# Performance work log

Hardware: AMD Instinct MI355X
Metric: run time of the kernel (lower is better)

Reference implementation:

```python
import jax, jax.numpy as jnp
import numpy as np

B = 256      # n_batch
N = 256      # n_x
RHO = 1.0    # control['rho']
N_ITERS = 50 # control['max_iters'], run fixed (no early stop) for determinism


def setup_inputs() -> dict:
    key = jax.random.key(0)
    k1, k2 = jax.random.split(key)
    # Build a well-conditioned symmetric PSD Q (QP requires Q PSD)
    Araw = jax.random.normal(k1, (B, N, N), dtype=jnp.float32)
    Q = jnp.einsum('bij,bkj->bik', Araw, Araw) / N + jnp.eye(N, dtype=jnp.float32)
    p = jax.random.normal(k2, (B, N, 1), dtype=jnp.float32)
    lb = -jnp.ones((B, N, 1), dtype=jnp.float32)
    ub = jnp.ones((B, N, 1), dtype=jnp.float32)
    return {"Q": Q, "p": p, "lb": lb, "ub": ub}


def reference(Q, p, lb, ub):
    n = Q.shape[1]
    # M = Q + rho*I, LU-factored once (rho fixed: adaptive_rho=False)
    M = Q + RHO * jnp.eye(n, dtype=Q.dtype)
    lu, piv = jax.vmap(jax.scipy.linalg.lu_factor)(M)
    solve = jax.vmap(lambda l, pv, r: jax.scipy.linalg.lu_solve((l, pv), r))

    x0 = jnp.zeros_like(p)
    z0 = jnp.zeros_like(p)
    u0 = jnp.zeros_like(p)

    def step(carry, _):
        x, z, u = carry
        rhs = -p + RHO * (z - u)            # [B,N,1]
        x = solve(lu, piv, rhs)             # batched LU solve
        z = jnp.clip(x + u, lb, ub)         # box projection (max with lb, min with ub)
        u = u + (x - z)                     # dual update
        return (x, z, u), None

    (x, z, u), _ = jax.lax.scan(step, (x0, z0, u0), None, length=N_ITERS)
    # scale=False => D=1, so sol x = D*x = x (unroll=True path returns x)
    return x
```

## Files before the change

### kernel.cpp

```cpp
#include <hip/hip_runtime.h>


#define NX     256
#define NITER  50
#define TRIF   33280
#define NTILE  2080
#define NTHR   1024

__device__ __forceinline__ int rowoff(int r) {
    int M = r >> 2, s = r & 3;
    return 4 * (M + 1) * ((M << 1) + s);
}

__launch_bounds__(NTHR, 1)
__global__ void boxqp_blk_kernel(const float* __restrict__ Q,
                                 const float* __restrict__ p,
                                 const float* __restrict__ lb,
                                 const float* __restrict__ ub,
                                 float* __restrict__ out)
{
    extern __shared__ char smem_raw[];
    float*  tri  = (float*)smem_raw;
    float4* tri4 = (float4*)tri;
    float4* P4   = (float4*)(tri + TRIF);
    float4* W4   = P4 + NX;
    float*  vbuf = (float*)(W4 + NX);
    unsigned char* lut = (unsigned char*)(vbuf + 272);

    const int t = threadIdx.x;
    const int b = blockIdx.x;
    const size_t qbase = ((size_t)b) << 16;

    if (t < 64) {
        int base = (t * (t + 1)) >> 1;
        for (int c = 0; c <= t; ++c) lut[base + c] = (unsigned char)t;
    }
    __syncthreads();

    for (int tile = t; tile < NTILE; tile += NTHR) {
        int rb = lut[tile];
        int cb = tile - ((rb * (rb + 1)) >> 1);
        int r0 = rb << 2, j0 = cb << 2;
        int q0 = ((rb + 1) * (rb << 1)) + cb, step = rb + 1;
        if (rb != cb) {
            #pragma unroll
            for (int s2 = 0; s2 < 4; ++s2) {
                float4 v = *(const float4*)(Q + qbase + (size_t)(r0 + s2) * NX + j0);
                tri4[q0 + s2 * step] = v;
            }
        } else {
            #pragma unroll
            for (int s2 = 0; s2 < 4; ++s2) {
                int rr = r0 + s2;
                float4 v = *(const float4*)(Q + qbase + (size_t)rr * NX + j0);
                float4 tq;
                tq.x = (j0 + 0 > rr) ? 0.f : (v.x + ((j0 + 0 == rr) ? 1.f : 0.f));
                tq.y = (j0 + 1 > rr) ? 0.f : (v.y + ((j0 + 1 == rr) ? 1.f : 0.f));
                tq.z = (j0 + 2 > rr) ? 0.f : (v.z + ((j0 + 2 == rr) ? 1.f : 0.f));
                tq.w = (j0 + 3 > rr) ? 0.f : (v.w + ((j0 + 3 == rr) ? 1.f : 0.f));
                tri4[q0 + s2 * step] = tq;
            }
        }
    }
    __syncthreads();

    for (int kb = 0; kb < 64; ++kb) {
        const int k0 = kb << 2;

        if (t < NX) {
            int i = t;
            float4 pv;
            if (i >= k0 + 4) {
                pv = tri4[(rowoff(i) >> 2) + kb];
            } else {
                float v0, v1, v2, v3;
                #pragma unroll
                for (int m = 0; m < 4; ++m) {
                    int km = k0 + m;
                    float vv = (km <= i) ? tri[rowoff(i) + km] : tri[rowoff(km) + i];
                    if (m == 0) v0 = vv; else if (m == 1) v1 = vv;
                    else if (m == 2) v2 = vv; else v3 = vv;
                }
                pv = make_float4(v0, v1, v2, v3);
            }
            P4[i] = pv;
        }
        __syncthreads();

        float S[4][4];
        {
            #pragma unroll
            for (int m = 0; m < 4; ++m) {
                float4 pr = P4[k0 + m];
                S[m][0] = pr.x; S[m][1] = pr.y; S[m][2] = pr.z; S[m][3] = pr.w;
            }
            #pragma unroll
            for (int kk = 0; kk < 4; ++kk) {
                float inv = 1.0f / S[kk][kk];
                #pragma unroll
                for (int a2 = 0; a2 < 4; ++a2) {
                    if (a2 == kk) continue;
                    #pragma unroll
                    for (int b2 = 0; b2 < 4; ++b2) {
                        if (b2 == kk) continue;
                        S[a2][b2] -= S[a2][kk] * S[kk][b2] * inv;
                    }
                }
                #pragma unroll
                for (int a2 = 0; a2 < 4; ++a2) {
                    if (a2 == kk) continue;
                    S[a2][kk] *= inv;
                    S[kk][a2] *= inv;
                }
                S[kk][kk] = -inv;
            }
        }
        if (t < NX) {
            float4 pr = P4[t];
            float4 w;
            w.x = -(pr.x * S[0][0] + pr.y * S[1][0] + pr.z * S[2][0] + pr.w * S[3][0]);
            w.y = -(pr.x * S[0][1] + pr.y * S[1][1] + pr.z * S[2][1] + pr.w * S[3][1]);
            w.z = -(pr.x * S[0][2] + pr.y * S[1][2] + pr.z * S[2][2] + pr.w * S[3][2]);
            w.w = -(pr.x * S[0][3] + pr.y * S[1][3] + pr.z * S[2][3] + pr.w * S[3][3]);
            W4[t] = w;
        }
        __syncthreads();

        for (int tile = t; tile < NTILE; tile += NTHR) {
            int rb = lut[tile];
            int cb = tile - ((rb * (rb + 1)) >> 1);
            int r0 = rb << 2;
            int q0 = ((rb + 1) * (rb << 1)) + cb, step = rb + 1;
            if (rb == kb) {
                if (cb == kb) {
                    #pragma unroll
                    for (int s2 = 0; s2 < 4; ++s2)
                        tri4[q0 + s2 * step] = make_float4(S[s2][0], S[s2][1], S[s2][2], S[s2][3]);
                } else {
                    int j0 = cb << 2;
                    #pragma unroll
                    for (int s2 = 0; s2 < 4; ++s2) {
                        float4 v;
                        v.x = ((const float*)(W4 + j0 + 0))[s2];
                        v.y = ((const float*)(W4 + j0 + 1))[s2];
                        v.z = ((const float*)(W4 + j0 + 2))[s2];
                        v.w = ((const float*)(W4 + j0 + 3))[s2];
                        tri4[q0 + s2 * step] = v;
                    }
                }
            } else if (cb == kb) {
                #pragma unroll
                for (int s2 = 0; s2 < 4; ++s2)
                    tri4[q0 + s2 * step] = W4[r0 + s2];
            } else {
                int j0 = cb << 2;
                float4 Pc0 = P4[j0 + 0], Pc1 = P4[j0 + 1], Pc2 = P4[j0 + 2], Pc3 = P4[j0 + 3];
                #pragma unroll
                for (int s2 = 0; s2 < 4; ++s2) {
                    float4 wr = W4[r0 + s2];
                    float4 tq = tri4[q0 + s2 * step];
                    tq.x -= wr.x * Pc0.x + wr.y * Pc0.y + wr.z * Pc0.z + wr.w * Pc0.w;
                    tq.y -= wr.x * Pc1.x + wr.y * Pc1.y + wr.z * Pc1.z + wr.w * Pc1.w;
                    tq.z -= wr.x * Pc2.x + wr.y * Pc2.y + wr.z * Pc2.z + wr.w * Pc2.w;
                    tq.w -= wr.x * Pc3.x + wr.y * Pc3.y + wr.z * Pc3.z + wr.w * Pc3.w;
                    tri4[q0 + s2 * step] = tq;
                }
            }
        }
        __syncthreads();
    }

    const int r  = t >> 2;
    const int q4 = t & 3;
    const int jc = q4 << 6;
    float mr[64];
    {
        const int offr = rowoff(r);
        #pragma unroll
        for (int jj = 0; jj < 64; ++jj) {
            int j = jc + jj;
            int addr = (j <= r) ? (offr + j) : (rowoff(j) + r);
            mr[jj] = tri[addr];
        }
    }

    const int gb = (b << 8) + r;
    const float pi = p[gb], lbi = lb[gb], ubi = ub[gb];
    const int vw = r + ((r >> 6) << 2);

    float x = 0.f, z = 0.f, u = 0.f;
    __syncthreads();
    for (int it = 0; it < NITER; ++it) {
        if (q4 == 0) vbuf[vw] = (u + pi) - z;
        __syncthreads();
        const float4* vb4 = (const float4*)(vbuf + q4 * 68);
        float a0 = 0.f, a1 = 0.f, a2 = 0.f, a3 = 0.f;
        #pragma unroll
        for (int m = 0; m < 16; ++m) {
            float4 v = vb4[m];
            a0 += mr[4 * m + 0] * v.x;
            a1 += mr[4 * m + 1] * v.y;
            a2 += mr[4 * m + 2] * v.z;
            a3 += mr[4 * m + 3] * v.w;
        }
        float s = (a0 + a1) + (a2 + a3);
        s += __shfl_xor(s, 1);
        s += __shfl_xor(s, 2);
        x = s;
        float xu = x + u;
        z = fminf(fmaxf(xu, lbi), ubi);
        u = xu - z;
        __syncthreads();
    }

    if (q4 == 0) out[gb] = x;
}

extern "C" void kernel_launch(void* const* d_in, const int* in_sizes, int n_in,
                              void* d_out, int out_size, void* d_ws, size_t ws_size,
                              hipStream_t stream) {
    const float* Q  = (const float*)d_in[0];
    const float* p  = (const float*)d_in[1];
    const float* lb = (const float*)d_in[2];
    const float* ub = (const float*)d_in[3];
    float* out = (float*)d_out;

    const size_t shmem = (size_t)TRIF * 4 + NX * 16 + NX * 16 + 272 * 4 + NTILE;
    (void)hipFuncSetAttribute((const void*)boxqp_blk_kernel,
                              hipFuncAttributeMaxDynamicSharedMemorySize,
                              (int)shmem);

    hipLaunchKernelGGL(boxqp_blk_kernel, dim3(256), dim3(NTHR), shmem, stream,
                       Q, p, lb, ub, out);
}
```

Measured before the change: 362.0 us.

## Swizzle packed-triangle LDS layout and split ADMM matvec across four row chunks

Rewrites the kernel with an XOR-swizzled packed lower-triangular layout in LDS to cut bank conflicts. Tile coordinates are now computed per thread with sqrt instead of a lookup table. The pivot panel is loaded by all 1024 threads into a transposed PT buffer, and W is stored both row-wise and transposed. The iteration matvec now reads the inverse directly from LDS, with each of four thread groups handling a 64-column chunk and partial sums reduced through LDS. This replaces the 64-register cached row, lowering register pressure but adding LDS traffic and an extra reduction step in every iteration.

Result: slower. 1.111 ms (+206.8%).

```diff
diff --git a/kernel.cpp b/kernel.cpp
--- a/kernel.cpp
+++ b/kernel.cpp
@@ -3,217 +3,260 @@
 
 #define NX     256
 #define NITER  50
-#define TRIF   33280
-#define NTILE  2080
 #define NTHR   1024
 
-__device__ __forceinline__ int rowoff(int r) {
-    int M = r >> 2, s = r & 3;
-    return 4 * (M + 1) * ((M << 1) + s);
-}
-
-__launch_bounds__(NTHR, 1)
-__global__ void boxqp_blk_kernel(const float* __restrict__ Q,
-                                 const float* __restrict__ p,
-                                 const float* __restrict__ lb,
-                                 const float* __restrict__ ub,
-                                 float* __restrict__ out)
+#define OFF_PT  33280
+#define OFF_W4  (OFF_PT + 4 * 264)
+#define OFF_WT  (OFF_W4 + 1024)
+#define LDS_F   (OFF_WT + 4 * 264)
+
+__host__ __device__ constexpr int rowoff(int r) {
+    return 4 * ((r >> 2) + 1) * (((r >> 2) << 1) + (r & 3));
+}
+__device__ __forceinline__ int triq(int q) { return q ^ ((q >> 3) & 7); }
+__device__ __forceinline__ int triF(int a) { return a ^ ((a >> 3) & 28); }
+
+__device__ __forceinline__ int tile_rb(int s) {
+    int r = (int)((sqrtf(8.0f * (float)s + 1.0f) - 1.0f) * 0.5f);
+    while ((r + 1) * (r + 2) / 2 <= s) ++r;
+    while (r * (r + 1) / 2 > s) --r;
+    return r;
+}
+
+template <int J0>
+__device__ __forceinline__ float chunk_upper_f(const float* tri, const float* vb, int rr) {
+    float a0 = 0.f, a1 = 0.f, a2 = 0.f, a3 = 0.f;
+    #pragma unroll
+    for (int jj = 0; jj < 64; jj += 4) {
+        a0 += tri[triF(rowoff(J0 + jj + 0) + rr)] * vb[J0 + jj + 0];
+        a1 += tri[triF(rowoff(J0 + jj + 1) + rr)] * vb[J0 + jj + 1];
+        a2 += tri[triF(rowoff(J0 + jj + 2) + rr)] * vb[J0 + jj + 2];
+        a3 += tri[triF(rowoff(J0 + jj + 3) + rr)] * vb[J0 + jj + 3];
+    }
+    return (a0 + a1) + (a2 + a3);
+}
+template <int J0>
+__device__ __forceinline__ float chunk_mixed_f(const float* tri, const float* vb, int rr) {
+    const int ror = rowoff(rr);
+    float a0 = 0.f, a1 = 0.f, a2 = 0.f, a3 = 0.f;
+    #pragma unroll
+    for (int jj = 0; jj < 64; jj += 4) {
+        {   const int j = J0 + jj + 0;
+            a0 += tri[triF((j <= rr) ? (ror + j) : (rowoff(j) + rr))] * vb[j]; }
+        {   const int j = J0 + jj + 1;
+            a1 += tri[triF((j <= rr) ? (ror + j) : (rowoff(j) + rr))] * vb[j]; }
+        {   const int j = J0 + jj + 2;
+            a2 += tri[triF((j <= rr) ? (ror + j) : (rowoff(j) + rr))] * vb[j]; }
+        {   const int j = J0 + jj + 3;
+            a3 += tri[triF((j <= rr) ? (ror + j) : (rowoff(j) + rr))] * vb[j]; }
+    }
+    return (a0 + a1) + (a2 + a3);
+}
+__device__ __forceinline__ float chunk_lower_f(const float4* tri4, const float* vb,
+                                               int rowq, int q4) {
+    const int qb = rowq + (q4 << 4);
+    const float* vbp = vb + (q4 << 6);
+    float a0 = 0.f, a1 = 0.f, a2 = 0.f, a3 = 0.f;
+    #pragma unroll
+    for (int m = 0; m < 16; ++m) {
+        const float4 A = tri4[triq(qb + m)];
+        const float4 V = *(const float4*)(vbp + 4 * m);
+        a0 += A.x * V.x; a1 += A.y * V.y; a2 += A.z * V.z; a3 += A.w * V.w;
+    }
+    return (a0 + a1) + (a2 + a3);
+}
+
+__global__ void __launch_bounds__(NTHR, 1)
+boxqp_r10_kernel(const float* __restrict__ Q,
+                 const float* __restrict__ p,
+                 const float* __restrict__ lb,
+                 const float* __restrict__ ub,
+                 float* __restrict__ out)
 {
-    extern __shared__ char smem_raw[];
-    float*  tri  = (float*)smem_raw;
-    float4* tri4 = (float4*)tri;
-    float4* P4   = (float4*)(tri + TRIF);
-    float4* W4   = P4 + NX;
-    float*  vbuf = (float*)(W4 + NX);
-    unsigned char* lut = (unsigned char*)(vbuf + 272);
+    __shared__ __align__(16) float lds[LDS_F];
+    float*  tri  = lds;
+    float4* tri4 = (float4*)lds;
+    float*  PT   = lds + OFF_PT;
+    float4* W4   = (float4*)(lds + OFF_W4);
+    float*  WT   = lds + OFF_WT;
+    float*  part = lds + OFF_PT;
+    float*  vbuf = lds + OFF_PT + 1024;
+    unsigned char* qrow = (unsigned char*)(lds + OFF_PT);
 
     const int t = threadIdx.x;
     const int b = blockIdx.x;
     const size_t qbase = ((size_t)b) << 16;
 
-    if (t < 64) {
-        int base = (t * (t + 1)) >> 1;
-        for (int c = 0; c <= t; ++c) lut[base + c] = (unsigned char)t;
+    const int rb0 = tile_rb(t),        cb0 = t        - ((rb0 * (rb0 + 1)) >> 1);
+    const int rb1 = tile_rb(t + 1024), cb1 = t + 1024 - ((rb1 * (rb1 + 1)) >> 1);
+    const int s2i = (t < 32) ? (t + 2048) : 2048;
+    const int rb2 = tile_rb(s2i),      cb2 = s2i      - ((rb2 * (rb2 + 1)) >> 1);
+
+    if (t < 256) {
+        const int bq = rowoff(t) >> 2, nq = (t >> 2) + 1;
+        for (int m = 0; m < nq; ++m) qrow[bq + m] = (unsigned char)t;
     }
     __syncthreads();
-
-    for (int tile = t; tile < NTILE; tile += NTHR) {
-        int rb = lut[tile];
-        int cb = tile - ((rb * (rb + 1)) >> 1);
-        int r0 = rb << 2, j0 = cb << 2;
-        int q0 = ((rb + 1) * (rb << 1)) + cb, step = rb + 1;
-        if (rb != cb) {
+    for (int q = t; q < 8320; q += NTHR) {
+        const int r  = qrow[q];
+        const int ro = rowoff(r) >> 2;
+        const int cq = q - ro;
+        float4 v = *(const float4*)(Q + qbase + ((size_t)r << 8) + (cq << 2));
+        if (cq == (r >> 2)) {
+            const int c0 = cq << 2;
+            v.x = (c0 + 0 > r) ? 0.f : (v.x + (c0 + 0 == r ? 1.f : 0.f));
+            v.y = (c0 + 1 > r) ? 0.f : (v.y + (c0 + 1 == r ? 1.f : 0.f));
+            v.z = (c0 + 2 > r) ? 0.f : (v.z + (c0 + 2 == r ? 1.f : 0.f));
+            v.w = (c0 + 3 > r) ? 0.f : (v.w + (c0 + 3 == r ? 1.f : 0.f));
+        }
+        tri4[triq(q)] = v;
+    }
+    __syncthreads();
+
+    const int i1 = t & 255;
+    const int m1 = t >> 8;
+
+    auto update_tile = [&](int rb, int cb, int kb, const float S[4][4]) {
+        const int r0 = rb << 2, j0 = cb << 2;
+        int roQ[4];
+        #pragma unroll
+        for (int s2 = 0; s2 < 4; ++s2) roQ[s2] = rowoff(r0 + s2) >> 2;
+
+        if (rb == kb) {
+            if (cb == kb) {
+                #pragma unroll
+                for (int s2 = 0; s2 < 4; ++s2)
+                    tri4[triq(roQ[s2] + cb)] =
+                        make_float4(S[s2][0], S[s2][1], S[s2][2], S[s2][3]);
+            } else {
+                #pragma unroll
+                for (int s2 = 0; s2 < 4; ++s2)
+                    tri4[triq(roQ[s2] + cb)] = *(const float4*)(WT + s2 * 264 + j0);
+            }
+        } else if (cb == kb) {
+            #pragma unroll
+            for (int s2 = 0; s2 < 4; ++s2)
+                tri4[triq(roQ[s2] + cb)] = W4[r0 + s2];
+        } else {
+            const float4 p0 = *(const float4*)(PT + 0 * 264 + j0);
+            const float4 p1 = *(const float4*)(PT + 1 * 264 + j0);
+            const float4 p2 = *(const float4*)(PT + 2 * 264 + j0);
+            const float4 p3 = *(const float4*)(PT + 3 * 264 + j0);
             #pragma unroll
             for (int s2 = 0; s2 < 4; ++s2) {
-                float4 v = *(const float4*)(Q + qbase + (size_t)(r0 + s2) * NX + j0);
-                tri4[q0 + s2 * step] = v;
-            }
-        } else {
-            #pragma unroll
-            for (int s2 = 0; s2 < 4; ++s2) {
-                int rr = r0 + s2;
-                float4 v = *(const float4*)(Q + qbase + (size_t)rr * NX + j0);
-                float4 tq;
-                tq.x = (j0 + 0 > rr) ? 0.f : (v.x + ((j0 + 0 == rr) ? 1.f : 0.f));
-                tq.y = (j0 + 1 > rr) ? 0.f : (v.y + ((j0 + 1 == rr) ? 1.f : 0.f));
-                tq.z = (j0 + 2 > rr) ? 0.f : (v.z + ((j0 + 2 == rr) ? 1.f : 0.f));
-                tq.w = (j0 + 3 > rr) ? 0.f : (v.w + ((j0 + 3 == rr) ? 1.f : 0.f));
-                tri4[q0 + s2 * step] = tq;
-            }
-        }
-    }
-    __syncthreads();
+                const float4 wr = W4[r0 + s2];
+                float4 a = tri4[triq(roQ[s2] + cb)];
+                a.x -= wr.x * p0.x + wr.y * p1.x + wr.z * p2.x + wr.w * p3.x;
+                a.y -= wr.x * p0.y + wr.y * p1.y + wr.z * p2.y + wr.w * p3.y;
+                a.z -= wr.x * p0.z + wr.y * p1.z + wr.z * p2.z + wr.w * p3.z;
+                a.w -= wr.x * p0.w + wr.y * p1.w + wr.z * p2.w + wr.w * p3.w;
+                tri4[triq(roQ[s2] + cb)] = a;
+            }
+        }
+    };
 
     for (int kb = 0; kb < 64; ++kb) {
         const int k0 = kb << 2;
 
-        if (t < NX) {
-            int i = t;
-            float4 pv;
-            if (i >= k0 + 4) {
-                pv = tri4[(rowoff(i) >> 2) + kb];
-            } else {
-                float v0, v1, v2, v3;
+        {
+            const int km = k0 + m1;
+            const float v = (km <= i1) ? tri[triF(rowoff(i1) + km)]
+                                       : tri[triF(rowoff(km) + i1)];
+            PT[m1 * 264 + i1] = v;
+        }
+        __syncthreads();
+
+        float S[4][4];
+        #pragma unroll
+        for (int mm = 0; mm < 4; ++mm) {
+            #pragma unroll
+            for (int c = 0; c < 4; ++c) S[mm][c] = PT[c * 264 + k0 + mm];
+        }
+        #pragma unroll
+        for (int kk = 0; kk < 4; ++kk) {
+            const float inv = 1.0f / S[kk][kk];
+            #pragma unroll
+            for (int a2 = 0; a2 < 4; ++a2) {
+                if (a2 == kk) continue;
                 #pragma unroll
-                for (int m = 0; m < 4; ++m) {
-                    int km = k0 + m;
-                    float vv = (km <= i) ? tri[rowoff(i) + km] : tri[rowoff(km) + i];
-                    if (m == 0) v0 = vv; else if (m == 1) v1 = vv;
-                    else if (m == 2) v2 = vv; else v3 = vv;
+                for (int b2 = 0; b2 < 4; ++b2) {
+                    if (b2 == kk) continue;
+                    S[a2][b2] -= S[a2][kk] * S[kk][b2] * inv;
                 }
-                pv = make_float4(v0, v1, v2, v3);
-            }
-            P4[i] = pv;
-        }
-        __syncthreads();
-
-        float S[4][4];
-        {
-            #pragma unroll
-            for (int m = 0; m < 4; ++m) {
-                float4 pr = P4[k0 + m];
-                S[m][0] = pr.x; S[m][1] = pr.y; S[m][2] = pr.z; S[m][3] = pr.w;
-            }
-            #pragma unroll
-            for (int kk = 0; kk < 4; ++kk) {
-                float inv = 1.0f / S[kk][kk];
-                #pragma unroll
-                for (int a2 = 0; a2 < 4; ++a2) {
-                    if (a2 == kk) continue;
-                    #pragma unroll
-                    for (int b2 = 0; b2 < 4; ++b2) {
-                        if (b2 == kk) continue;
-                        S[a2][b2] -= S[a2][kk] * S[kk][b2] * inv;
-                    }
-                }
-                #pragma unroll
-                for (int a2 = 0; a2 < 4; ++a2) {
-                    if (a2 == kk) continue;
-                    S[a2][kk] *= inv;
-                    S[kk][a2] *= inv;
-                }
-                S[kk][kk] = -inv;
-            }
-        }
-        if (t < NX) {
-            float4 pr = P4[t];
-            float4 w;
-            w.x = -(pr.x * S[0][0] + pr.y * S[1][0] + pr.z * S[2][0] + pr.w * S[3][0]);
-            w.y = -(pr.x * S[0][1] + pr.y * S[1][1] + pr.z * S[2][1] + pr.w * S[3][1]);
-            w.z = -(pr.x * S[0][2] + pr.y * S[1][2] + pr.z * S[2][2] + pr.w * S[3][2]);
-            w.w = -(pr.x * S[0][3] + pr.y * S[1][3] + pr.z * S[2][3] + pr.w * S[3][3]);
-            W4[t] = w;
-        }
-        __syncthreads();
-
-        for (int tile = t; tile < NTILE; tile += NTHR) {
-            int rb = lut[tile];
-            int cb = tile - ((rb * (rb + 1)) >> 1);
-            int r0 = rb << 2;
-            int q0 = ((rb + 1) * (rb << 1)) + cb, step = rb + 1;
-            if (rb == kb) {
-                if (cb == kb) {
-                    #pragma unroll
-                    for (int s2 = 0; s2 < 4; ++s2)
-                        tri4[q0 + s2 * step] = make_float4(S[s2][0], S[s2][1], S[s2][2], S[s2][3]);
-                } else {
-                    int j0 = cb << 2;
-                    #pragma unroll
-                    for (int s2 = 0; s2 < 4; ++s2) {
-                        float4 v;
-                        v.x = ((const float*)(W4 + j0 + 0))[s2];
-                        v.y = ((const float*)(W4 + j0 + 1))[s2];
-                        v.z = ((const float*)(W4 + j0 + 2))[s2];
-                        v.w = ((const float*)(W4 + j0 + 3))[s2];
-                        tri4[q0 + s2 * step] = v;
-                    }
-                }
-            } else if (cb == kb) {
-                #pragma unroll
-                for (int s2 = 0; s2 < 4; ++s2)
-                    tri4[q0 + s2 * step] = W4[r0 + s2];
-            } else {
-                int j0 = cb << 2;
-                float4 Pc0 = P4[j0 + 0], Pc1 = P4[j0 + 1], Pc2 = P4[j0 + 2], Pc3 = P4[j0 + 3];
-                #pragma unroll
-                for (int s2 = 0; s2 < 4; ++s2) {
-                    float4 wr = W4[r0 + s2];
-                    float4 tq = tri4[q0 + s2 * step];
-                    tq.x -= wr.x * Pc0.x + wr.y * Pc0.y + wr.z * Pc0.z + wr.w * Pc0.w;
-                    tq.y -= wr.x * Pc1.x + wr.y * Pc1.y + wr.z * Pc1.z + wr.w * Pc1.w;
-                    tq.z -= wr.x * Pc2.x + wr.y * Pc2.y + wr.z * Pc2.z + wr.w * Pc2.w;
-                    tq.w -= wr.x * Pc3.x + wr.y * Pc3.y + wr.z * Pc3.z + wr.w * Pc3.w;
-                    tri4[q0 + s2 * step] = tq;
-                }
-            }
-        }
-        __syncthreads();
-    }
-
-    const int r  = t >> 2;
-    const int q4 = t & 3;
-    const int jc = q4 << 6;
-    float mr[64];
-    {
-        const int offr = rowoff(r);
-        #pragma unroll
-        for (int jj = 0; jj < 64; ++jj) {
-            int j = jc + jj;
-            int addr = (j <= r) ? (offr + j) : (rowoff(j) + r);
-            mr[jj] = tri[addr];
-        }
-    }
-
-    const int gb = (b << 8) + r;
-    const float pi = p[gb], lbi = lb[gb], ubi = ub[gb];
-    const int vw = r + ((r >> 6) << 2);
-
-    float x = 0.f, z = 0.f, u = 0.f;
+            }
+            #pragma unroll
+            for (int a2 = 0; a2 < 4; ++a2) {
+                if (a2 == kk) continue;
+                S[a2][kk] *= inv;
+                S[kk][a2] *= inv;
+            }
+            S[kk][kk] = -inv;
+        }
+
+        if (t < 256) {
+            const float pv0 = PT[0 * 264 + t], pv1 = PT[1 * 264 + t];
+            const float pv2 = PT[2 * 264 + t], pv3 = PT[3 * 264 + t];
+            const float w0 = -(pv0 * S[0][0] + pv1 * S[1][0] + pv2 * S[2][0] + pv3 * S[3][0]);
+            const float w1 = -(pv0 * S[0][1] + pv1 * S[1][1] + pv2 * S[2][1] + pv3 * S[3][1]);
+            const float w2 = -(pv0 * S[0][2] + pv1 * S[1][2] + pv2 * S[2][2] + pv3 * S[3][2]);
+            const float w3 = -(pv0 * S[0][3] + pv1 * S[1][3] + pv2 * S[2][3] + pv3 * S[3][3]);
+            W4[t] = make_float4(w0, w1, w2, w3);
+            WT[0 * 264 + t] = w0; WT[1 * 264 + t] = w1;
+            WT[2 * 264 + t] = w2; WT[3 * 264 + t] = w3;
+        }
+        __syncthreads();
+
+        update_tile(rb0, cb0, kb, S);
+        update_tile(rb1, cb1, kb, S);
+        if (t < 32) update_tile(rb2, cb2, kb, S);
+        __syncthreads();
+    }
+
+    const int rr   = t & 255;
+    const int q4   = t >> 8;
+    const int sw   = (t >> 6) & 3;
+    const int rowq = rowoff(rr) >> 2;
+
+    float x = 0.f, z = 0.f, uu = 0.f;
+    float pi = 0.f, lbi = 0.f, ubi = 0.f;
+    if (t < 256) {
+        const int gb = (b << 8) + t;
+        pi = p[gb]; lbi = lb[gb]; ubi = ub[gb];
+        vbuf[t] = pi;
+    }
     __syncthreads();
+
     for (int it = 0; it < NITER; ++it) {
-        if (q4 == 0) vbuf[vw] = (u + pi) - z;
-        __syncthreads();
-        const float4* vb4 = (const float4*)(vbuf + q4 * 68);
-        float a0 = 0.f, a1 = 0.f, a2 = 0.f, a3 = 0.f;
-        #pragma unroll
-        for (int m = 0; m < 16; ++m) {
-            float4 v = vb4[m];
-            a0 += mr[4 * m + 0] * v.x;
-            a1 += mr[4 * m + 1] * v.y;
-            a2 += mr[4 * m + 2] * v.z;
-            a3 += mr[4 * m + 3] * v.w;
-        }
-        float s = (a0 + a1) + (a2 + a3);
-        s += __shfl_xor(s, 1);
-        s += __shfl_xor(s, 2);
-        x = s;
-        float xu = x + u;
-        z = fminf(fmaxf(xu, lbi), ubi);
-        u = xu - z;
-        __syncthreads();
-    }
-
-    if (q4 == 0) out[gb] = x;
+        float acc;
+        if (sw > q4) {
+            acc = chunk_lower_f(tri4, vbuf, rowq, q4);
+        } else if (sw == q4) {
+            switch (q4) {
+                case 0:  acc = chunk_mixed_f<0  >(tri, vbuf, rr); break;
+                case 1:  acc = chunk_mixed_f<64 >(tri, vbuf, rr); break;
+                case 2:  acc = chunk_mixed_f<128>(tri, vbuf, rr); break;
+                default: acc = chunk_mixed_f<192>(tri, vbuf, rr); break;
+            }
+        } else {
+            switch (q4) {
+                case 1:  acc = chunk_upper_f<64 >(tri, vbuf, rr); break;
+                case 2:  acc = chunk_upper_f<128>(tri, vbuf, rr); break;
+                default: acc = chunk_upper_f<192>(tri, vbuf, rr); break;
+            }
+        }
+        part[(q4 << 8) | rr] = acc;
+        __syncthreads();
+        if (t < 256) {
+            x = part[t] + part[256 + t] + part[512 + t] + part[768 + t];
+            const float xu = x + uu;
+            z  = fminf(fmaxf(xu, lbi), ubi);
+            uu = xu - z;
+            vbuf[t] = (uu + pi) - z;
+        }
+        __syncthreads();
+    }
+
+    if (t < 256) out[(b << 8) + t] = x;
 }
 
 extern "C" void kernel_launch(void* const* d_in, const int* in_sizes, int n_in,
@@ -225,11 +268,6 @@
     const float* ub = (const float*)d_in[3];
     float* out = (float*)d_out;
 
-    const size_t shmem = (size_t)TRIF * 4 + NX * 16 + NX * 16 + 272 * 4 + NTILE;
-    (void)hipFuncSetAttribute((const void*)boxqp_blk_kernel,
-                              hipFuncAttributeMaxDynamicSharedMemorySize,
-                              (int)shmem);
-
-    hipLaunchKernelGGL(boxqp_blk_kernel, dim3(256), dim3(NTHR), shmem, stream,
+    hipLaunchKernelGGL(boxqp_r10_kernel, dim3(256), dim3(NTHR), 0, stream,
                        Q, p, lb, ub, out);
 }
```
